# Performance work log

Measured on AMD Instinct MI355X. Metric: run time of the kernel, lower is better.

Reference implementation:

```python
import jax, jax.numpy as jnp
import numpy as np

OUT, IN, B = 11008, 4096, 32

def setup_inputs() -> dict:
    key = jax.random.key(0)
    k1, k2, k3, k4 = jax.random.split(key, 4)
    x = jax.random.normal(k1, (B, IN), dtype=jnp.float32)
    # ternary weights in {-1, 0, +1}, stored as int (int8 semantics)
    weight_q = jax.random.randint(k2, (OUT, IN), -1, 2, dtype=jnp.int32)
    # per-row positive scale (fp16 in torch, cast to fp32 at dequant time)
    weight_scale = jax.random.uniform(k3, (OUT, 1), dtype=jnp.float32, minval=0.01, maxval=1.0)
    bias = jax.random.normal(k4, (OUT,), dtype=jnp.float32)
    return {"x": x, "weight_q": weight_q, "weight_scale": weight_scale, "bias": bias}

def reference(x, weight_q, weight_scale, bias):
    # dequantize_2bit: int8 ternary * per-row scale -> fp32 weight [OUT, IN]
    W = weight_q.astype(jnp.float32) * weight_scale.astype(jnp.float32)
    # F.linear: x @ W.T + bias
    return jnp.einsum('bi,oi->bo', x.astype(jnp.float32), W) + bias
```

## Files before the change

kernel.cpp:

```cpp
#include <hip/hip_runtime.h>

#define OUT_N 11008
#define IN_K  4096
#define BATCH 32
#define NO    256
#define KB    32
#define SEGS  32
#define KC    (IN_K / SEGS)

__global__ __launch_bounds__(256) void prep_kernel(
    const float* __restrict__ x, const float* __restrict__ bias,
    float* __restrict__ xT, float* __restrict__ out)
{
    int i = blockIdx.x * 256 + threadIdx.x;
    if (i < BATCH * IN_K) {
        int b = i >> 12;
        int k = i & (IN_K - 1);
        xT[k * BATCH + b] = x[i];
    }
    if (i < BATCH * OUT_N) {
        int o = i % OUT_N;
        out[i] = bias[o];
    }
}

__global__ __launch_bounds__(256, 4) void lin2bit_kernel(
    const int* __restrict__ wq, const float* __restrict__ scale,
    const float* __restrict__ xT, float* __restrict__ out)
{
    __shared__ float lw[KB][NO + 1];

    const int t    = threadIdx.x;
    const int o0   = blockIdx.x * NO;
    const int kseg = blockIdx.y * KC;
    const int o    = o0 + t;

    float acc[BATCH];
#pragma unroll
    for (int b = 0; b < BATCH; ++b) acc[b] = 0.f;

    for (int chunk = 0; chunk < KC / KB; ++chunk) {
        const int k0 = kseg + chunk * KB;

#pragma unroll
        for (int j = 0; j < 8; ++j) {
            const int r = j * 32 + (t >> 3);
            const int c = (t & 7) * 4;
            const int4 v = *reinterpret_cast<const int4*>(
                wq + (size_t)(o0 + r) * IN_K + k0 + c);
            lw[c + 0][r] = (float)v.x;
            lw[c + 1][r] = (float)v.y;
            lw[c + 2][r] = (float)v.z;
            lw[c + 3][r] = (float)v.w;
        }
        __syncthreads();

        const float* __restrict__ xr = xT + (size_t)k0 * BATCH;
#pragma unroll 8
        for (int k = 0; k < KB; ++k) {
            const float w = lw[k][t];
#pragma unroll
            for (int b = 0; b < BATCH; ++b)
                acc[b] = fmaf(xr[k * BATCH + b], w, acc[b]);
        }
        __syncthreads();
    }

    const float s = scale[o];
#pragma unroll
    for (int b = 0; b < BATCH; ++b) {
        unsafeAtomicAdd(out + (size_t)b * OUT_N + o, s * acc[b]);
    }
}

extern "C" void kernel_launch(void* const* d_in, const int* in_sizes, int n_in,
                              void* d_out, int out_size, void* d_ws, size_t ws_size,
                              hipStream_t stream) {
    const float* x     = (const float*)d_in[0];
    const int*   wq    = (const int*)d_in[1];
    const float* scale = (const float*)d_in[2];
    const float* bias  = (const float*)d_in[3];
    float* out = (float*)d_out;
    float* xT  = (float*)d_ws;

    prep_kernel<<<dim3((BATCH * OUT_N + 255) / 256), 256, 0, stream>>>(x, bias, xT, out);
    lin2bit_kernel<<<dim3(OUT_N / NO, SEGS), 256, 0, stream>>>(wq, scale, xT, out);
}
```

Baseline: 297.3 us.

## Use bf16 MFMA with x staged in LDS for ternary linear

Replaces the scalar FMA loop with 16x16x32 bf16 MFMA instructions. Weights are converted from int32 to bf16 in registers, and x is pre-rounded to bf16 in the prep kernel and staged per K-segment in shared memory. The work decomposition changes to 64 outputs per block and 8 K segments, which reduces the number of atomic adds. Rounding activations to bf16 costs precision, but accumulation stays in fp32.

```diff
diff --git a/kernel.cpp b/kernel.cpp
--- a/kernel.cpp
+++ b/kernel.cpp
@@ -3,73 +3,91 @@
 #define OUT_N 11008
 #define IN_K  4096
 #define BATCH 32
-#define NO    256
-#define KB    32
-#define SEGS  32
-#define KC    (IN_K / SEGS)
+#define SEGS  8
+#define KSEG  (IN_K / SEGS)
+#define OPB   64
+#define XSTRIDE 520
+
+typedef __attribute__((ext_vector_type(8))) short short8;
+typedef __attribute__((ext_vector_type(4))) float float4v;
 
 __global__ __launch_bounds__(256) void prep_kernel(
     const float* __restrict__ x, const float* __restrict__ bias,
-    float* __restrict__ xT, float* __restrict__ out)
+    unsigned short* __restrict__ xb, float* __restrict__ out)
 {
     int i = blockIdx.x * 256 + threadIdx.x;
     if (i < BATCH * IN_K) {
-        int b = i >> 12;
-        int k = i & (IN_K - 1);
-        xT[k * BATCH + b] = x[i];
+        unsigned u = __builtin_bit_cast(unsigned, x[i]);
+        unsigned r = u + 0x7FFFu + ((u >> 16) & 1u);
+        xb[i] = (unsigned short)(r >> 16);
     }
     if (i < BATCH * OUT_N) {
-        int o = i % OUT_N;
-        out[i] = bias[o];
+        out[i] = bias[i % OUT_N];
     }
+}
+
+__device__ __forceinline__ unsigned pkbf16(float fhi, float flo) {
+    return __builtin_amdgcn_perm(__builtin_bit_cast(unsigned, fhi),
+                                 __builtin_bit_cast(unsigned, flo),
+                                 0x07060302u);
 }
 
 __global__ __launch_bounds__(256, 4) void lin2bit_kernel(
     const int* __restrict__ wq, const float* __restrict__ scale,
-    const float* __restrict__ xT, float* __restrict__ out)
+    const unsigned short* __restrict__ xb, float* __restrict__ out)
 {
-    __shared__ float lw[KB][NO + 1];
+    __shared__ unsigned short xs[BATCH][XSTRIDE];
 
     const int t    = threadIdx.x;
-    const int o0   = blockIdx.x * NO;
-    const int kseg = blockIdx.y * KC;
-    const int o    = o0 + t;
-
-    float acc[BATCH];
-#pragma unroll
-    for (int b = 0; b < BATCH; ++b) acc[b] = 0.f;
-
-    for (int chunk = 0; chunk < KC / KB; ++chunk) {
-        const int k0 = kseg + chunk * KB;
+    const int lane = t & 63;
+    const int wave = t >> 6;
+    const int kseg = blockIdx.y * KSEG;
 
 #pragma unroll
-        for (int j = 0; j < 8; ++j) {
-            const int r = j * 32 + (t >> 3);
-            const int c = (t & 7) * 4;
-            const int4 v = *reinterpret_cast<const int4*>(
-                wq + (size_t)(o0 + r) * IN_K + k0 + c);
-            lw[c + 0][r] = (float)v.x;
-            lw[c + 1][r] = (float)v.y;
-            lw[c + 2][r] = (float)v.z;
-            lw[c + 3][r] = (float)v.w;
-        }
-        __syncthreads();
+    for (int it = 0; it < 8; ++it) {
+        int idx = it * 256 + t;
+        int b   = idx >> 6;
+        int k8  = (idx & 63) * 8;
+        uint4 v = *reinterpret_cast<const uint4*>(xb + b * IN_K + kseg + k8);
+        *reinterpret_cast<uint4*>(&xs[b][k8]) = v;
+    }
+    __syncthreads();
 
-        const float* __restrict__ xr = xT + (size_t)k0 * BATCH;
-#pragma unroll 8
-        for (int k = 0; k < KB; ++k) {
-            const float w = lw[k][t];
-#pragma unroll
-            for (int b = 0; b < BATCH; ++b)
-                acc[b] = fmaf(xr[k * BATCH + b], w, acc[b]);
-        }
-        __syncthreads();
+    const int quad = lane >> 4;
+    const int l16  = lane & 15;
+    const int o    = blockIdx.x * OPB + wave * 16 + l16;
+
+    const int* __restrict__ wrow = wq + (size_t)o * IN_K + kseg + quad * 8;
+    const unsigned short* xrow0 = &xs[l16][quad * 8];
+    const unsigned short* xrow1 = &xs[l16 + 16][quad * 8];
+
+    float4v acc0 = {0.f, 0.f, 0.f, 0.f};
+    float4v acc1 = {0.f, 0.f, 0.f, 0.f};
+
+#pragma unroll 4
+    for (int ki = 0; ki < KSEG; ki += 32) {
+        int4 w0 = *reinterpret_cast<const int4*>(wrow + ki);
+        int4 w1 = *reinterpret_cast<const int4*>(wrow + ki + 4);
+        uint4 bwu;
+        bwu.x = pkbf16((float)w0.y, (float)w0.x);
+        bwu.y = pkbf16((float)w0.w, (float)w0.z);
+        bwu.z = pkbf16((float)w1.y, (float)w1.x);
+        bwu.w = pkbf16((float)w1.w, (float)w1.z);
+        short8 bfrag = __builtin_bit_cast(short8, bwu);
+
+        short8 a0 = *reinterpret_cast<const short8*>(xrow0 + ki);
+        short8 a1 = *reinterpret_cast<const short8*>(xrow1 + ki);
+
+        acc0 = __builtin_amdgcn_mfma_f32_16x16x32_bf16(a0, bfrag, acc0, 0, 0, 0);
+        acc1 = __builtin_amdgcn_mfma_f32_16x16x32_bf16(a1, bfrag, acc1, 0, 0, 0);
     }
 
     const float s = scale[o];
+    const int b0 = quad * 4;
 #pragma unroll
-    for (int b = 0; b < BATCH; ++b) {
-        unsafeAtomicAdd(out + (size_t)b * OUT_N + o, s * acc[b]);
+    for (int r = 0; r < 4; ++r) {
+        unsafeAtomicAdd(out + (size_t)(b0 + r)      * OUT_N + o, s * acc0[r]);
+        unsafeAtomicAdd(out + (size_t)(b0 + r + 16) * OUT_N + o, s * acc1[r]);
     }
 }
 
@@ -81,8 +99,8 @@
     const float* scale = (const float*)d_in[2];
     const float* bias  = (const float*)d_in[3];
     float* out = (float*)d_out;
-    float* xT  = (float*)d_ws;
+    unsigned short* xb = (unsigned short*)d_ws;
 
-    prep_kernel<<<dim3((BATCH * OUT_N + 255) / 256), 256, 0, stream>>>(x, bias, xT, out);
-    lin2bit_kernel<<<dim3(OUT_N / NO, SEGS), 256, 0, stream>>>(wq, scale, xT, out);
+    prep_kernel<<<dim3((BATCH * OUT_N + 255) / 256), 256, 0, stream>>>(x, bias, xb, out);
+    lin2bit_kernel<<<dim3(OUT_N / OPB, SEGS), 256, 0, stream>>>(wq, scale, xb, out);
 }
```

After: 256.3 us. 13.8% less time.
